# Optimization experiments

Hardware: AMD Instinct MI355X
Metric: run time of the kernel (lower is better)

## Reference

```python
import jax, jax.numpy as jnp
import numpy as np

B, V, J, NB, P = 1024, 6890, 24, 10, 207
PARENTS = np.array([-1, 0, 0, 0, 1, 2, 3, 4, 5, 6, 7, 8, 9, 9, 9, 12, 13, 14, 16, 17, 18, 19, 20, 21], dtype=np.int32)


def batch_rodrigues(rot_vecs):
    # rot_vecs: [N,3] axis-angle -> [N,3,3] rotation matrices (matches torch impl incl. +1e-8)
    angle = jnp.linalg.norm(rot_vecs + 1e-8, axis=1, keepdims=True)  # [N,1]
    rot_dir = rot_vecs / angle
    cos = jnp.cos(angle)[:, :, None]  # [N,1,1]
    sin = jnp.sin(angle)[:, :, None]
    rx, ry, rz = rot_dir[:, 0], rot_dir[:, 1], rot_dir[:, 2]
    zeros = jnp.zeros_like(rx)
    K = jnp.stack([zeros, -rz, ry, rz, zeros, -rx, -ry, rx, zeros], axis=1).reshape(-1, 3, 3)
    ident = jnp.eye(3, dtype=rot_vecs.dtype)[None]
    return ident + sin * K + (1.0 - cos) * jnp.matmul(K, K)


def batch_rigid_transform(rot_mats, joints):
    # rot_mats: [B,J,3,3], joints: [B,J,3]
    rel_joints = joints.at[:, 1:].add(-joints[:, PARENTS[1:]])
    top = jnp.concatenate([rot_mats, rel_joints[..., None]], axis=-1)  # [B,J,3,4]
    bottom = jnp.broadcast_to(jnp.array([0.0, 0.0, 0.0, 1.0], dtype=rot_mats.dtype), top.shape[:2] + (1, 4))
    transforms_mat = jnp.concatenate([top, bottom], axis=-2)  # [B,J,4,4]
    chain = [transforms_mat[:, 0]]
    for i in range(1, J):  # fixed 24-joint kinematic tree
        chain.append(jnp.matmul(chain[PARENTS[i]], transforms_mat[:, i]))
    transforms = jnp.stack(chain, axis=1)  # [B,J,4,4]
    posed_joints = transforms[:, :, :3, 3]
    # rel_transforms = transforms - pad(transforms @ [j;0]) : subtract rotated rest joint from last column
    tj = jnp.einsum('bjmk,bjk->bjm', transforms[..., :3], joints)  # [B,J,4]
    rel_transforms = transforms.at[..., 3].add(-tj)
    return posed_joints, rel_transforms


def reference(betas, poses, extra_joints_idxs, v_template, shapedirs, posedirs, J_regressor, lbs_weights, J_regressor_extra9, J_regressor_h36m17):
    b = betas.shape[0]
    v_shaped = v_template + jnp.einsum('bl,vkl->bvk', betas, shapedirs)  # [B,V,3]
    Jrest = jnp.einsum('bvk,jv->bjk', v_shaped, J_regressor)  # [B,J,3]
    rot_mats = batch_rodrigues(poses.reshape(-1, 3)).reshape(b, J, 3, 3)
    ident = jnp.eye(3, dtype=poses.dtype)
    pose_feature = (rot_mats[:, 1:] - ident).reshape(b, -1)  # [B,207]
    pose_offsets = jnp.matmul(pose_feature, posedirs).reshape(b, V, 3)
    v_posed = pose_offsets + v_shaped
    J_transformed, A = batch_rigid_transform(rot_mats, Jrest)
    # blend skinning: T = W @ A, then transform homogeneous vertices
    T = jnp.einsum('vj,bjmn->bvmn', lbs_weights, A)  # [B,V,4,4]
    verts = jnp.einsum('bvmk,bvk->bvm', T[:, :, :3, :3], v_posed) + T[:, :, :3, 3]
    extra11 = verts[:, extra_joints_idxs]  # [B,11,3]
    extra9 = jnp.einsum('bvk,jv->bjk', verts, J_regressor_extra9)
    h36m17 = jnp.einsum('bvk,jv->bjk', verts, J_regressor_h36m17)
    joints44_17 = jnp.concatenate([J_transformed, extra11, extra9, h36m17], axis=1)  # [B,61,3]
    return verts, joints44_17


def setup_inputs():
    key = jax.random.key(0)
    ks = jax.random.split(key, 10)
    betas = jax.random.normal(ks[0], (B, NB), dtype=jnp.float32)
    poses = jax.random.normal(ks[1], (B, J * 3), dtype=jnp.float32) * 0.3
    v_template = jax.random.normal(ks[2], (V, 3), dtype=jnp.float32)
    shapedirs = jax.random.normal(ks[3], (V, 3, NB), dtype=jnp.float32) * 0.01
    posedirs = jax.random.normal(ks[4], (P, V * 3), dtype=jnp.float32) * 0.01
    Jr = jax.random.uniform(ks[5], (J, V), dtype=jnp.float32)
    J_regressor = Jr / jnp.sum(Jr, axis=1, keepdims=True)
    Wl = jax.random.uniform(ks[6], (V, J), dtype=jnp.float32)
    lbs_weights = Wl / jnp.sum(Wl, axis=1, keepdims=True)
    Je9 = jax.random.uniform(ks[7], (9, V), dtype=jnp.float32)
    J_regressor_extra9 = Je9 / jnp.sum(Je9, axis=1, keepdims=True)
    Jh = jax.random.uniform(ks[8], (17, V), dtype=jnp.float32)
    J_regressor_h36m17 = Jh / jnp.sum(Jh, axis=1, keepdims=True)
    extra_joints_idxs = jax.random.randint(ks[9], (11,), 0, V, dtype=jnp.int32)
    return {'betas': betas, 'poses': poses, 'extra_joints_idxs': extra_joints_idxs,
            'v_template': v_template, 'shapedirs': shapedirs, 'posedirs': posedirs,
            'J_regressor': J_regressor, 'lbs_weights': lbs_weights,
            'J_regressor_extra9': J_regressor_extra9, 'J_regressor_h36m17': J_regressor_h36m17}
```

## Files before the change

kernel.cpp:

```cpp
#include <hip/hip_runtime.h>

#define VV 6890
#define N3 20670
#define NVT 216
#define NKC 7
#define NJOUT 61
#define OUTJ ((size_t)1024*VV*3)
#define NJCH 216
#define NSEG 27

#define WS_JT 0
#define WS_JS 72
#define WS_JALL_BYTES 4096
#define WS_ABLK_BYTES 1183744
#define WS_BBLK_BYTES 1642496
#define WS_A2_BYTES   10932224
#define WS_W2_BYTES   12505088

typedef float f32x4 __attribute__((ext_vector_type(4)));
typedef short bf16x8 __attribute__((ext_vector_type(8)));

__constant__ int c_par[24] = {-1,0,0,0,1,2,3,4,5,6,7,8,9,9,9,12,13,14,16,17,18,19,20,21};

__device__ __forceinline__ short f2bf(float x) {
    union { float f; unsigned u; } v; v.f = x;
    unsigned r = (v.u + 0x7fffu + ((v.u >> 16) & 1u)) >> 16;
    return (short)r;
}
__device__ __forceinline__ float bf2f(short h) {
    union { unsigned u; float f; } v; v.u = ((unsigned)(unsigned short)h) << 16;
    return v.f;
}

__global__ __launch_bounds__(256) void k_prep(
    const float* __restrict__ pd, const float* __restrict__ sd,
    const float* __restrict__ lbsw, const float* __restrict__ Je9,
    const float* __restrict__ Jh, const float* __restrict__ Jreg,
    const float* __restrict__ vt,
    short* __restrict__ Bblk, short* __restrict__ W2, short* __restrict__ JallF,
    float* __restrict__ ws)
{
    const int bid = blockIdx.x;
    const int tid = threadIdx.x;
    __shared__ float T[32][97];

    if (bid < 1512) {
        const int nt = bid / 7, kc = bid % 7;
        for (int idx = tid; idx < 3072; idx += 256) {
            const int kl = idx / 96, c = idx % 96;
            const int kg = kc*32 + kl;
            const int n = nt*96 + c;
            float val = 0.f;
            if (n < N3) {
                if (kg < 207) val = pd[(size_t)kg*N3 + n];
                else if (kg < 217) val = sd[(size_t)(n/3)*30 + (n%3)*10 + (kg-207)];
            }
            T[kl][c] = val;
        }
        __syncthreads();
        short* tile = Bblk + (size_t)(nt*NKC + kc)*3072;
        for (int s = tid; s < 384; s += 256) {
            const int c = s >> 2;
            const int hi = (s & 3) ^ ((c >> 1) & 3);
            bf16x8 pk;
#pragma unroll
            for (int e = 0; e < 8; e++) pk[e] = f2bf(T[hi*8+e][c]);
            *(bf16x8*)(tile + s*8) = pk;
        }
    } else if (bid < 1944) {
        if (tid < 64) {
            const int l = tid;
            const int l15 = l & 15, l4 = l >> 4;
            const int sb = bid - 1512;
            if (sb < NVT) {
                const int nt = sb;
#pragma unroll
                for (int nh = 0; nh < 2; nh++) {
                    const int v = nt*32 + nh*16 + l15;
                    bf16x8 pk;
#pragma unroll
                    for (int q = 0; q < 8; q++) {
                        const int j = l4*8 + q;
                        float val = (j < 24 && v < VV) ? lbsw[(size_t)v*24 + j] : 0.f;
                        pk[q] = f2bf(val);
                    }
                    *(bf16x8*)(W2 + ((size_t)(nt*2 + nh)*512) + l*8) = pk;
                }
            } else {
                const int ch = sb - NVT;
#pragma unroll
                for (int jh = 0; jh < 2; jh++) {
                    const int j = jh*16 + l15;
                    bf16x8 pk;
#pragma unroll
                    for (int q = 0; q < 8; q++) {
                        const int v = ch*32 + l4*8 + q;
                        float val = 0.f;
                        if (j < 26 && v < VV)
                            val = (j < 9) ? Je9[(size_t)j*VV + v] : Jh[(size_t)(j-9)*VV + v];
                        pk[q] = f2bf(val);
                    }
                    *(bf16x8*)(JallF + ((size_t)ch*2 + jh)*512 + l*8) = pk;
                }
            }
        }
    } else {
        const int jb = bid - 1944;
        const int j = jb / 3, k = jb % 3;
        float acc[11];
#pragma unroll
        for (int i = 0; i < 11; i++) acc[i] = 0.f;
        for (int v = tid; v < VV; v += 256) {
            const float jr = Jreg[j*VV + v];
            acc[0] += jr * vt[v*3 + k];
            const float* s = sd + (size_t)v*30 + k*10;
#pragma unroll
            for (int l = 0; l < 10; l++) acc[1+l] += jr * s[l];
        }
#pragma unroll
        for (int off = 1; off < 64; off <<= 1)
#pragma unroll
            for (int i = 0; i < 11; i++) acc[i] += __shfl_xor(acc[i], off);
        const int wv = tid >> 6, ln = tid & 63;
        if (ln == 0)
#pragma unroll
            for (int i = 0; i < 11; i++) T[wv][i] = acc[i];
        __syncthreads();
        if (tid == 0) {
            ws[WS_JT + j*3 + k] = T[0][0]+T[1][0]+T[2][0]+T[3][0];
#pragma unroll
            for (int l = 0; l < 10; l++)
                ws[WS_JS + (j*3+k)*10 + l] = T[0][1+l]+T[1][1+l]+T[2][1+l]+T[3][1+l];
        }
    }
}

__global__ __launch_bounds__(64) void k_batch(
    const float* __restrict__ betas, const float* __restrict__ poses,
    float* __restrict__ ws, short* __restrict__ Ablk, short* __restrict__ A2,
    float* __restrict__ out)
{
    const int b = blockIdx.x, lane = threadIdx.x;
    __shared__ float R[24][9], Jr[24][3], RJ[24][3], G[24][12];
    if (lane < 24) {
        const int j = lane;
        const float x = poses[b*72 + j*3 + 0];
        const float y = poses[b*72 + j*3 + 1];
        const float z = poses[b*72 + j*3 + 2];
        const float xe = x + 1e-8f, ye = y + 1e-8f, ze = z + 1e-8f;
        const float ang = sqrtf(xe*xe + ye*ye + ze*ze);
        const float inv = 1.0f / ang;
        const float rx = x*inv, ry = y*inv, rz = z*inv;
        const float sn = sinf(ang), cs = cosf(ang);
        const float K[9] = {0.f,-rz,ry, rz,0.f,-rx, -ry,rx,0.f};
        float Rl[9];
#pragma unroll
        for (int r = 0; r < 3; r++)
#pragma unroll
            for (int c = 0; c < 3; c++) {
                float kk = 0.f;
#pragma unroll
                for (int m = 0; m < 3; m++) kk += K[r*3+m]*K[m*3+c];
                Rl[r*3+c] = ((r==c)?1.f:0.f) + sn*K[r*3+c] + (1.f-cs)*kk;
            }
#pragma unroll
        for (int e = 0; e < 9; e++) R[j][e] = Rl[e];
#pragma unroll
        for (int k = 0; k < 3; k++) {
            float a = ws[WS_JT + j*3 + k];
#pragma unroll
            for (int l = 0; l < 10; l++) a += betas[b*10 + l] * ws[WS_JS + (j*3+k)*10 + l];
            Jr[j][k] = a;
        }
    }
    __syncthreads();
    {
        const int r = b & 31, mt = b >> 5;
        const int sw = (r >> 1) & 3;
        for (int k = lane; k < 224; k += 64) {
            float val;
            if (k < 207) { const int j = k/9 + 1, e = k - (j-1)*9;
                           val = R[j][e] - ((e==0||e==4||e==8)?1.f:0.f); }
            else if (k < 217) val = betas[b*10 + (k-207)];
            else val = 0.f;
            const int kc = k >> 5, hi = (k >> 3) & 3;
            Ablk[(size_t)(mt*NKC + kc)*1024 + r*32 + ((hi ^ sw)*8) + (k & 7)] = f2bf(val);
        }
    }
    if (lane < 24) {
        const int j = lane, p = c_par[j];
#pragma unroll
        for (int k = 0; k < 3; k++) RJ[j][k] = (j == 0) ? Jr[0][k] : (Jr[j][k] - Jr[p][k]);
    }
    __syncthreads();
    if (lane < 12) {
        const int r = lane >> 2, c = lane & 3;
        G[0][lane] = (c < 3) ? R[0][r*3+c] : RJ[0][r];
    }
    __syncthreads();
    for (int i = 1; i < 24; i++) {
        float val = 0.f;
        if (lane < 12) {
            const int r = lane >> 2, c = lane & 3, p = c_par[i];
            if (c < 3)
                val = G[p][r*4+0]*R[i][0+c] + G[p][r*4+1]*R[i][3+c] + G[p][r*4+2]*R[i][6+c];
            else
                val = G[p][r*4+0]*RJ[i][0] + G[p][r*4+1]*RJ[i][1] + G[p][r*4+2]*RJ[i][2] + G[p][r*4+3];
        }
        __syncthreads();
        if (lane < 12) G[i][lane] = val;
        __syncthreads();
    }
    if (lane < 24)
#pragma unroll
        for (int k = 0; k < 3; k++)
            out[OUTJ + ((size_t)b*NJOUT + lane)*3 + k] = G[lane][k*4+3];
    const int bt = b >> 5, mh = (b >> 4) & 1, b15 = b & 15;
    short* A2t = A2 + (size_t)bt*12*2*2*512;
    for (int e = lane; e < 288; e += 64) {
        const int j = e / 12, rc = e % 12, r = rc >> 2, c = rc & 3;
        float val = G[j][rc];
        if (c == 3)
            val -= G[j][r*4+0]*Jr[j][0] + G[j][r*4+1]*Jr[j][1] + G[j][r*4+2]*Jr[j][2];
        const short vhi = f2bf(val);
        const short vlo = f2bf(val - bf2f(vhi));
        const int lf = (j >> 3)*16 + b15, q = j & 7;
        A2t[((rc*2 + 0)*2 + mh)*512 + lf*8 + q] = vhi;
        A2t[((rc*2 + 1)*2 + mh)*512 + lf*8 + q] = vlo;
    }
    for (int idx = lane; idx < 192; idx += 64) {
        const int rc = idx >> 4, spl = (idx >> 3) & 1, q = idx & 7;
        A2t[((rc*2 + spl)*2 + mh)*512 + (48 + b15)*8 + q] = 0;
    }
}

__global__ __launch_bounds__(256, 3) void k_fused(
    const short* __restrict__ Ablk, const short* __restrict__ Bblk,
    const short* __restrict__ A2, const short* __restrict__ W2,
    const float* __restrict__ vt, float* __restrict__ out)
{
    const int nt = blockIdx.x, bt = blockIdx.y;
    const int tid = threadIdx.x;
    const int lane = tid & 63, wid = tid >> 6;
    const int wm = wid >> 1, wn = wid & 1;
    const int l15 = lane & 15, l4 = lane >> 4;

    __shared__ char SM[41984] __attribute__((aligned(16)));
    float*  Tl16 = (float*)SM;
    float*  vp   = (float*)(SM + 25088);

    const int e_base = wid*3;
    bf16x8 a2f[3][2][2], w2f[2];
    {
        const short* A2t = A2 + (size_t)bt*12*2*2*512;
#pragma unroll
        for (int ee = 0; ee < 3; ee++)
#pragma unroll
            for (int mh = 0; mh < 2; mh++)
#pragma unroll
                for (int spl = 0; spl < 2; spl++)
                    a2f[ee][mh][spl] = *(const bf16x8*)(A2t + (((e_base+ee)*2 + spl)*2 + mh)*512 + lane*8);
#pragma unroll
        for (int nh = 0; nh < 2; nh++)
            w2f[nh] = *(const bf16x8*)(W2 + (size_t)(nt*2 + nh)*512 + lane*8);
    }

    f32x4 acc[3];
#pragma unroll
    for (int n = 0; n < 3; n++) acc[n] = (f32x4){0.f,0.f,0.f,0.f};
    const int ar = wm*16 + l15;
    const int aoff = ar*32 + ((l4 ^ ((ar >> 1) & 3)) * 8);
    int boff[3];
#pragma unroll
    for (int n = 0; n < 3; n++) {
        const int c = wn*48 + n*16 + l15;
        boff[n] = c*32 + ((l4 ^ ((c >> 1) & 3)) * 8);
    }
    const short* gA = Ablk + (size_t)bt*NKC*1024;
    const short* gB = Bblk + (size_t)nt*NKC*3072;

#pragma unroll
    for (int kc = 0; kc < NKC; kc++) {
        const bf16x8 af  = *(const bf16x8*)(gA + kc*1024 + aoff);
        const bf16x8 bf0 = *(const bf16x8*)(gB + kc*3072 + boff[0]);
        const bf16x8 bf1 = *(const bf16x8*)(gB + kc*3072 + boff[1]);
        const bf16x8 bf2 = *(const bf16x8*)(gB + kc*3072 + boff[2]);
        acc[0] = __builtin_amdgcn_mfma_f32_16x16x32_bf16(af, bf0, acc[0], 0, 0, 0);
        acc[1] = __builtin_amdgcn_mfma_f32_16x16x32_bf16(af, bf1, acc[1], 0, 0, 0);
        acc[2] = __builtin_amdgcn_mfma_f32_16x16x32_bf16(af, bf2, acc[2], 0, 0, 0);
    }

#pragma unroll
    for (int n = 0; n < 3; n++) {
        const int cl = wn*48 + n*16 + l15;
        const int cg = nt*96 + cl;
        const float vtv = (cg < N3) ? vt[cg] : 0.f;
        const int vloc = cl / 3, kk = cl - vloc*3;
        const int b0 = wm*16 + l4*4;
#pragma unroll
        for (int rg = 0; rg < 4; rg++)
            vp[(b0+rg)*132 + vloc*4 + kk] = acc[n][rg] + vtv;
    }

    f32x4 at[3][2][2];
#pragma unroll
    for (int ee = 0; ee < 3; ee++)
#pragma unroll
        for (int mh = 0; mh < 2; mh++)
#pragma unroll
            for (int nh = 0; nh < 2; nh++) {
                f32x4 t = (f32x4){0.f,0.f,0.f,0.f};
                t = __builtin_amdgcn_mfma_f32_16x16x32_bf16(a2f[ee][mh][0], w2f[nh], t, 0, 0, 0);
                t = __builtin_amdgcn_mfma_f32_16x16x32_bf16(a2f[ee][mh][1], w2f[nh], t, 0, 0, 0);
                at[ee][mh][nh] = t;
            }

#pragma unroll
    for (int half = 0; half < 2; half++) {
#pragma unroll
        for (int ee = 0; ee < 3; ee++)
#pragma unroll
            for (int mh = 0; mh < 2; mh++) {
                const int brow = mh*16 + l4*4;
#pragma unroll
                for (int rg = 0; rg < 4; rg++)
                    Tl16[(brow+rg)*196 + (e_base+ee)*16 + l15] = at[ee][mh][half][rg];
            }
        __syncthreads();
        const int bl = tid >> 3, vq = tid & 7;
        const int bg = bt*32 + bl;
#pragma unroll
        for (int i = 0; i < 2; i++) {
            const int v = vq + 8*i;
            const float4 u = *(const float4*)&vp[bl*132 + (half*16 + v)*4];
            float t[12];
#pragma unroll
            for (int e = 0; e < 12; e++) t[e] = Tl16[bl*196 + e*16 + v];
            const float r0 = t[0]*u.x + t[1]*u.y + t[2]*u.z  + t[3];
            const float r1 = t[4]*u.x + t[5]*u.y + t[6]*u.z  + t[7];
            const float r2 = t[8]*u.x + t[9]*u.y + t[10]*u.z + t[11];
            const int gv = nt*32 + half*16 + v;
            if (gv < VV) {
                const size_t base = (size_t)bg*N3 + (size_t)gv*3;
                out[base+0] = r0; out[base+1] = r1; out[base+2] = r2;
            }
        }
        if (half == 0) __syncthreads();
    }
}

__global__ __launch_bounds__(256) void k_jreg2(
    const float* __restrict__ vsrc, const short* __restrict__ JallF,
    float* __restrict__ P)
{
    const int bt = blockIdx.x, seg = blockIdx.y;
    const int tid = threadIdx.x;
    const int lane = tid & 63, wid = tid >> 6;
    const int jh = wid >> 1, nh = wid & 1;
    const int l15 = lane & 15, l4 = lane >> 4;

    f32x4 C[3];
#pragma unroll
    for (int k = 0; k < 3; k++) C[k] = (f32x4){0.f,0.f,0.f,0.f};

    const int rowb = bt*32 + nh*16 + l15;
    const float* vrow = vsrc + (size_t)rowb*N3;
    const int c0 = seg*8, c1 = c0 + 8;
    for (int ch = c0; ch < c1; ch++) {
        const float* p = vrow + ch*96 + l4*24;
        float2 g[12];
#pragma unroll
        for (int t = 0; t < 12; t++) g[t] = *(const float2*)(p + t*2);
        const bf16x8 af = *(const bf16x8*)(JallF + ((size_t)ch*2 + jh)*512 + lane*8);
#pragma unroll
        for (int k = 0; k < 3; k++) {
            bf16x8 bf;
#pragma unroll
            for (int q = 0; q < 8; q++) {
                const int e = q*3 + k;
                bf[q] = f2bf((e & 1) ? g[e>>1].y : g[e>>1].x);
            }
            C[k] = __builtin_amdgcn_mfma_f32_16x16x32_bf16(af, bf, C[k], 0, 0, 0);
        }
    }
    float* Pp = P + (size_t)(seg*32 + bt)*2496 + (nh*16 + l15)*78;
#pragma unroll
    for (int k = 0; k < 3; k++)
#pragma unroll
        for (int rg = 0; rg < 4; rg++) {
            const int j = jh*16 + l4*4 + rg;
            if (j < 26) Pp[j*3 + k] = C[k][rg];
        }
}

__global__ __launch_bounds__(256) void k_tail(
    const float* __restrict__ P, const int* __restrict__ eidx, float* __restrict__ out)
{
    const int gid = blockIdx.x*256 + threadIdx.x;
    if (gid < 79872) {
        const int b = gid / 78, r = gid % 78;
        float s = 0.f;
#pragma unroll
        for (int seg = 0; seg < NSEG; seg++)
            s += P[(size_t)(seg*32 + (b >> 5))*2496 + (b & 31)*78 + r];
        out[OUTJ + (size_t)b*183 + 105 + r] = s;
    } else if (gid < 79872 + 33792) {
        const int idx = gid - 79872;
        const int b = idx / 33, r = idx % 33, j = r / 3, k = r % 3;
        out[OUTJ + ((size_t)b*NJOUT + 24 + j)*3 + k] =
            out[(size_t)b*N3 + (size_t)eidx[j]*3 + k];
    }
}

extern "C" void kernel_launch(void* const* d_in, const int* in_sizes, int n_in,
                              void* d_out, int out_size, void* d_ws, size_t ws_size,
                              hipStream_t stream) {
    const float* betas = (const float*)d_in[0];
    const float* poses = (const float*)d_in[1];
    const int*   eidx  = (const int*)  d_in[2];
    const float* vt    = (const float*)d_in[3];
    const float* sd    = (const float*)d_in[4];
    const float* pd    = (const float*)d_in[5];
    const float* Jreg  = (const float*)d_in[6];
    const float* lbsw  = (const float*)d_in[7];
    const float* Je9   = (const float*)d_in[8];
    const float* Jh    = (const float*)d_in[9];
    float* out = (float*)d_out;
    float* ws  = (float*)d_ws;
    short* JallF = (short*)((char*)d_ws + WS_JALL_BYTES);
    short* Ablk  = (short*)((char*)d_ws + WS_ABLK_BYTES);
    short* Bblk  = (short*)((char*)d_ws + WS_BBLK_BYTES);
    short* A2    = (short*)((char*)d_ws + WS_A2_BYTES);
    short* W2    = (short*)((char*)d_ws + WS_W2_BYTES);
    float* Pprt  = (float*)((char*)d_ws + WS_BBLK_BYTES);

    k_prep  <<<dim3(2016),      dim3(256), 0, stream>>>(pd, sd, lbsw, Je9, Jh, Jreg, vt,
                                                        Bblk, W2, JallF, ws);
    k_batch <<<dim3(1024),      dim3(64),  0, stream>>>(betas, poses, ws, Ablk, A2, out);
    k_fused <<<dim3(NVT, 32),   dim3(256), 0, stream>>>(Ablk, Bblk, A2, W2, vt, out);
    k_jreg2 <<<dim3(32, NSEG),  dim3(256), 0, stream>>>(out, JallF, Pprt);
    k_tail  <<<dim3(444),       dim3(256), 0, stream>>>(Pprt, eidx, out);
}
```

Before: 106.1 us.

## Process two vertex tiles per block in fused LBS kernel

Each k_fused block now handles two adjacent vertex tiles (nt0, nt1). This reuses the A fragments and the per-batch A2 transform fragments across both tiles, and halves the grid to 108x32. The aim is to cut redundant A/A2 loads and per-block setup. In exchange it uses more shared memory and registers, lowers launch bounds occupancy to 2 blocks, and launches fewer blocks.

New measurement: 121.3 us. 14.3% more time.

```diff
diff --git a/kernel.cpp b/kernel.cpp
--- a/kernel.cpp
+++ b/kernel.cpp
@@ -234,23 +234,25 @@
     }
 }
 
-__global__ __launch_bounds__(256, 3) void k_fused(
+__global__ __launch_bounds__(256, 2) void k_fused(
     const short* __restrict__ Ablk, const short* __restrict__ Bblk,
     const short* __restrict__ A2, const short* __restrict__ W2,
     const float* __restrict__ vt, float* __restrict__ out)
 {
-    const int nt = blockIdx.x, bt = blockIdx.y;
+    const int nt0 = blockIdx.x*2, nt1 = nt0 + 1;
+    const int bt = blockIdx.y;
     const int tid = threadIdx.x;
     const int lane = tid & 63, wid = tid >> 6;
     const int wm = wid >> 1, wn = wid & 1;
     const int l15 = lane & 15, l4 = lane >> 4;
 
-    __shared__ char SM[41984] __attribute__((aligned(16)));
+    __shared__ char SM[58880] __attribute__((aligned(16)));
     float*  Tl16 = (float*)SM;
-    float*  vp   = (float*)(SM + 25088);
+    float*  vp0  = (float*)(SM + 25088);
+    float*  vp1  = (float*)(SM + 41984);
 
     const int e_base = wid*3;
-    bf16x8 a2f[3][2][2], w2f[2];
+    bf16x8 a2f[3][2][2], w2f0[2], w2f1[2];
     {
         const short* A2t = A2 + (size_t)bt*12*2*2*512;
 #pragma unroll
@@ -261,13 +263,18 @@
                 for (int spl = 0; spl < 2; spl++)
                     a2f[ee][mh][spl] = *(const bf16x8*)(A2t + (((e_base+ee)*2 + spl)*2 + mh)*512 + lane*8);
 #pragma unroll
-        for (int nh = 0; nh < 2; nh++)
-            w2f[nh] = *(const bf16x8*)(W2 + (size_t)(nt*2 + nh)*512 + lane*8);
-    }
-
-    f32x4 acc[3];
-#pragma unroll
-    for (int n = 0; n < 3; n++) acc[n] = (f32x4){0.f,0.f,0.f,0.f};
+        for (int nh = 0; nh < 2; nh++) {
+            w2f0[nh] = *(const bf16x8*)(W2 + (size_t)(nt0*2 + nh)*512 + lane*8);
+            w2f1[nh] = *(const bf16x8*)(W2 + (size_t)(nt1*2 + nh)*512 + lane*8);
+        }
+    }
+
+    f32x4 acc0[3], acc1[3];
+#pragma unroll
+    for (int n = 0; n < 3; n++) {
+        acc0[n] = (f32x4){0.f,0.f,0.f,0.f};
+        acc1[n] = (f32x4){0.f,0.f,0.f,0.f};
+    }
     const int ar = wm*16 + l15;
     const int aoff = ar*32 + ((l4 ^ ((ar >> 1) & 3)) * 8);
     int boff[3];
@@ -276,76 +283,95 @@
         const int c = wn*48 + n*16 + l15;
         boff[n] = c*32 + ((l4 ^ ((c >> 1) & 3)) * 8);
     }
-    const short* gA = Ablk + (size_t)bt*NKC*1024;
-    const short* gB = Bblk + (size_t)nt*NKC*3072;
+    const short* gA  = Ablk + (size_t)bt*NKC*1024;
+    const short* gB0 = Bblk + (size_t)nt0*NKC*3072;
+    const short* gB1 = Bblk + (size_t)nt1*NKC*3072;
 
 #pragma unroll
     for (int kc = 0; kc < NKC; kc++) {
-        const bf16x8 af  = *(const bf16x8*)(gA + kc*1024 + aoff);
-        const bf16x8 bf0 = *(const bf16x8*)(gB + kc*3072 + boff[0]);
-        const bf16x8 bf1 = *(const bf16x8*)(gB + kc*3072 + boff[1]);
-        const bf16x8 bf2 = *(const bf16x8*)(gB + kc*3072 + boff[2]);
-        acc[0] = __builtin_amdgcn_mfma_f32_16x16x32_bf16(af, bf0, acc[0], 0, 0, 0);
-        acc[1] = __builtin_amdgcn_mfma_f32_16x16x32_bf16(af, bf1, acc[1], 0, 0, 0);
-        acc[2] = __builtin_amdgcn_mfma_f32_16x16x32_bf16(af, bf2, acc[2], 0, 0, 0);
+        const bf16x8 af = *(const bf16x8*)(gA + kc*1024 + aoff);
+#pragma unroll
+        for (int n = 0; n < 3; n++) {
+            const bf16x8 b0 = *(const bf16x8*)(gB0 + kc*3072 + boff[n]);
+            acc0[n] = __builtin_amdgcn_mfma_f32_16x16x32_bf16(af, b0, acc0[n], 0, 0, 0);
+        }
+#pragma unroll
+        for (int n = 0; n < 3; n++) {
+            const bf16x8 b1 = *(const bf16x8*)(gB1 + kc*3072 + boff[n]);
+            acc1[n] = __builtin_amdgcn_mfma_f32_16x16x32_bf16(af, b1, acc1[n], 0, 0, 0);
+        }
     }
 
 #pragma unroll
     for (int n = 0; n < 3; n++) {
         const int cl = wn*48 + n*16 + l15;
-        const int cg = nt*96 + cl;
-        const float vtv = (cg < N3) ? vt[cg] : 0.f;
         const int vloc = cl / 3, kk = cl - vloc*3;
         const int b0 = wm*16 + l4*4;
-#pragma unroll
-        for (int rg = 0; rg < 4; rg++)
-            vp[(b0+rg)*132 + vloc*4 + kk] = acc[n][rg] + vtv;
-    }
-
-    f32x4 at[3][2][2];
-#pragma unroll
-    for (int ee = 0; ee < 3; ee++)
-#pragma unroll
-        for (int mh = 0; mh < 2; mh++)
-#pragma unroll
-            for (int nh = 0; nh < 2; nh++) {
-                f32x4 t = (f32x4){0.f,0.f,0.f,0.f};
-                t = __builtin_amdgcn_mfma_f32_16x16x32_bf16(a2f[ee][mh][0], w2f[nh], t, 0, 0, 0);
-                t = __builtin_amdgcn_mfma_f32_16x16x32_bf16(a2f[ee][mh][1], w2f[nh], t, 0, 0, 0);
-                at[ee][mh][nh] = t;
+        {
+            const int cg = nt0*96 + cl;
+            const float vtv = (cg < N3) ? vt[cg] : 0.f;
+#pragma unroll
+            for (int rg = 0; rg < 4; rg++)
+                vp0[(b0+rg)*132 + vloc*4 + kk] = acc0[n][rg] + vtv;
+        }
+        {
+            const int cg = nt1*96 + cl;
+            const float vtv = (cg < N3) ? vt[cg] : 0.f;
+#pragma unroll
+            for (int rg = 0; rg < 4; rg++)
+                vp1[(b0+rg)*132 + vloc*4 + kk] = acc1[n][rg] + vtv;
+        }
+    }
+
+#pragma unroll
+    for (int part = 0; part < 2; part++) {
+        const int nt = part ? nt1 : nt0;
+        const float* vp = part ? vp1 : vp0;
+        f32x4 at[3][2][2];
+#pragma unroll
+        for (int ee = 0; ee < 3; ee++)
+#pragma unroll
+            for (int mh = 0; mh < 2; mh++)
+#pragma unroll
+                for (int nh = 0; nh < 2; nh++) {
+                    const bf16x8 w = part ? w2f1[nh] : w2f0[nh];
+                    f32x4 t = (f32x4){0.f,0.f,0.f,0.f};
+                    t = __builtin_amdgcn_mfma_f32_16x16x32_bf16(a2f[ee][mh][0], w, t, 0, 0, 0);
+                    t = __builtin_amdgcn_mfma_f32_16x16x32_bf16(a2f[ee][mh][1], w, t, 0, 0, 0);
+                    at[ee][mh][nh] = t;
+                }
+#pragma unroll
+        for (int half = 0; half < 2; half++) {
+#pragma unroll
+            for (int ee = 0; ee < 3; ee++)
+#pragma unroll
+                for (int mh = 0; mh < 2; mh++) {
+                    const int brow = mh*16 + l4*4;
+#pragma unroll
+                    for (int rg = 0; rg < 4; rg++)
+                        Tl16[(brow+rg)*196 + (e_base+ee)*16 + l15] = at[ee][mh][half][rg];
+                }
+            __syncthreads();
+            const int bl = tid >> 3, vq = tid & 7;
+            const int bg = bt*32 + bl;
+#pragma unroll
+            for (int i = 0; i < 2; i++) {
+                const int v = vq + 8*i;
+                const float4 u = *(const float4*)&vp[bl*132 + (half*16 + v)*4];
+                float t[12];
+#pragma unroll
+                for (int e = 0; e < 12; e++) t[e] = Tl16[bl*196 + e*16 + v];
+                const float r0 = t[0]*u.x + t[1]*u.y + t[2]*u.z  + t[3];
+                const float r1 = t[4]*u.x + t[5]*u.y + t[6]*u.z  + t[7];
+                const float r2 = t[8]*u.x + t[9]*u.y + t[10]*u.z + t[11];
+                const int gv = nt*32 + half*16 + v;
+                if (gv < VV) {
+                    const size_t base = (size_t)bg*N3 + (size_t)gv*3;
+                    out[base+0] = r0; out[base+1] = r1; out[base+2] = r2;
+                }
             }
-
-#pragma unroll
-    for (int half = 0; half < 2; half++) {
-#pragma unroll
-        for (int ee = 0; ee < 3; ee++)
-#pragma unroll
-            for (int mh = 0; mh < 2; mh++) {
-                const int brow = mh*16 + l4*4;
-#pragma unroll
-                for (int rg = 0; rg < 4; rg++)
-                    Tl16[(brow+rg)*196 + (e_base+ee)*16 + l15] = at[ee][mh][half][rg];
-            }
-        __syncthreads();
-        const int bl = tid >> 3, vq = tid & 7;
-        const int bg = bt*32 + bl;
-#pragma unroll
-        for (int i = 0; i < 2; i++) {
-            const int v = vq + 8*i;
-            const float4 u = *(const float4*)&vp[bl*132 + (half*16 + v)*4];
-            float t[12];
-#pragma unroll
-            for (int e = 0; e < 12; e++) t[e] = Tl16[bl*196 + e*16 + v];
-            const float r0 = t[0]*u.x + t[1]*u.y + t[2]*u.z  + t[3];
-            const float r1 = t[4]*u.x + t[5]*u.y + t[6]*u.z  + t[7];
-            const float r2 = t[8]*u.x + t[9]*u.y + t[10]*u.z + t[11];
-            const int gv = nt*32 + half*16 + v;
-            if (gv < VV) {
-                const size_t base = (size_t)bg*N3 + (size_t)gv*3;
-                out[base+0] = r0; out[base+1] = r1; out[base+2] = r2;
-            }
-        }
-        if (half == 0) __syncthreads();
+            if (!(part == 1 && half == 1)) __syncthreads();
+        }
     }
 }
 
@@ -437,7 +463,7 @@
     k_prep  <<<dim3(2016),      dim3(256), 0, stream>>>(pd, sd, lbsw, Je9, Jh, Jreg, vt,
                                                         Bblk, W2, JallF, ws);
     k_batch <<<dim3(1024),      dim3(64),  0, stream>>>(betas, poses, ws, Ablk, A2, out);
-    k_fused <<<dim3(NVT, 32),   dim3(256), 0, stream>>>(Ablk, Bblk, A2, W2, vt, out);
+    k_fused <<<dim3(108, 32),   dim3(256), 0, stream>>>(Ablk, Bblk, A2, W2, vt, out);
     k_jreg2 <<<dim3(32, NSEG),  dim3(256), 0, stream>>>(out, JallF, Pprt);
     k_tail  <<<dim3(444),       dim3(256), 0, stream>>>(Pprt, eidx, out);
 }
```
